# Optimization experiments

Hardware: AMD Instinct MI355X
Metric: run time of the kernel (lower is better)

Reference implementation:

```python
import jax, jax.numpy as jnp
import numpy as np

N_NODES = 100000
N_EDGES = 1600000
IN_DIM = 128
HID_DIM = 128
OUT_DIM = 64


def gcn_conv(x, W, b, edge_index):
    """GCNConv with add_self_loops, symmetric degree norm, add-aggregation.

    Math matches PyG: out[i] = sum_{(j,i) in E+selfloops} norm_ji * (x_j @ W) + b
    Since lin is linear and there is no edge_attr, we transform x once before
    the gather instead of per-edge (identical result, far less FLOPs/traffic).
    """
    n = x.shape[0]
    loop = jnp.arange(n, dtype=edge_index.dtype)
    row = jnp.concatenate([edge_index[0], loop])  # source nodes (x_j)
    col = jnp.concatenate([edge_index[1], loop])  # destination nodes
    # degree over destinations (includes self loops -> deg >= 1, no div by 0)
    deg = jax.ops.segment_sum(jnp.ones_like(col, dtype=x.dtype), col, num_segments=n)
    dinv = jax.lax.rsqrt(deg)
    norm = dinv[row] * dinv[col]  # [E+N]
    h = x @ W  # [N, out] transform once
    msg = norm[:, None] * h[row]  # [E+N, out] gathered per-edge messages
    out = jax.ops.segment_sum(msg, col, num_segments=n)  # scatter-add
    return out + b


def setup_inputs() -> dict:
    key = jax.random.key(0)
    k1, k2, k3, k4 = jax.random.split(key, 4)
    x = jax.random.normal(k1, (N_NODES, IN_DIM), dtype=jnp.float32)
    edge_index = jax.random.randint(k2, (2, N_EDGES), 0, N_NODES, dtype=jnp.int64)
    # glorot-ish init
    W1 = jax.random.normal(k3, (IN_DIM, HID_DIM), dtype=jnp.float32) * (2.0 / (IN_DIM + HID_DIM)) ** 0.5
    W2 = jax.random.normal(k4, (HID_DIM, OUT_DIM), dtype=jnp.float32) * (2.0 / (HID_DIM + OUT_DIM)) ** 0.5
    b1 = jnp.zeros((HID_DIM,), dtype=jnp.float32)
    b2 = jnp.zeros((OUT_DIM,), dtype=jnp.float32)
    return {"x": x, "edge_index": edge_index, "W1": W1, "b1": b1, "W2": W2, "b2": b2}


def reference(x, edge_index, W1, b1, W2, b2):
    # GCN.forward with prompt_type=None, pooling=False, eval mode (dropout is identity)
    h = gcn_conv(x, W1, b1, edge_index)
    h = jax.nn.relu(h)
    out = gcn_conv(h, W2, b2, edge_index)
    return out
```

## Files before the change

### kernel.cpp

```cpp
#include <hip/hip_runtime.h>


#define DIN 128
#define DHID 128
#define DOUT 64
#define ELLW 64
#define GPART 8
#define BPG 256

typedef __attribute__((ext_vector_type(4))) float f32x4;
typedef __attribute__((ext_vector_type(8))) short bf16x8;

__device__ __forceinline__ float bf2f(unsigned int u16) {
    return __uint_as_float(u16 << 16);
}
__device__ __forceinline__ unsigned short f2bf(float f) {
    unsigned int u = __float_as_uint(f);
    u += 0x7fffu + ((u >> 16) & 1u);
    return (unsigned short)(u >> 16);
}
__device__ __forceinline__ unsigned int pack2(float a, float b) {
    return (unsigned int)f2bf(a) | ((unsigned int)f2bf(b) << 16);
}

__global__ __launch_bounds__(256) void k_fill(const int* __restrict__ rows,
                                              const int* __restrict__ cols,
                                              int* __restrict__ deg,
                                              int* __restrict__ ell,
                                              int E, int perBlock, int R) {
    int g  = blockIdx.x & (GPART - 1);
    int cb = blockIdx.x >> 3;
    int lo = g * R, hi = lo + R;
    int eBeg = cb * perBlock;
    int eEnd = eBeg + perBlock; if (eEnd > E) eEnd = E;
    for (int e = eBeg + threadIdx.x; e < eEnd; e += 256) {
        int c = cols[e];
        if (c >= lo && c < hi) {
            int r = rows[e];
            int k = atomicAdd(&deg[c], 1);
            if (k < ELLW) ell[(size_t)c * ELLW + k] = r;
        }
    }
}

__global__ void k_dinv(const int* __restrict__ deg, float* __restrict__ dinv, int N) {
    int i = blockIdx.x * blockDim.x + threadIdx.x;
    if (i < N) dinv[i] = rsqrtf((float)(deg[i] + 1));
}

__global__ __launch_bounds__(256) void k_packW(const float* __restrict__ W1,
                                               const float* __restrict__ W2,
                                               unsigned short* __restrict__ w1p,
                                               unsigned short* __restrict__ w2p) {
    int id = blockIdx.x * 256 + threadIdx.x;
    if (id < 2048) {
        int lane = id & 63, s = (id >> 6) & 3, t = id >> 8;
        int n = t * 16 + (lane & 15);
        int k0 = s * 32 + (lane >> 4) * 8;
#pragma unroll
        for (int j = 0; j < 8; ++j)
            w1p[(size_t)id * 8 + j] = f2bf(W1[(k0 + j) * DHID + n]);
    } else if (id < 3072) {
        int id2 = id - 2048;
        int lane = id2 & 63, s = (id2 >> 6) & 3, t = id2 >> 8;
        int n = t * 16 + (lane & 15);
        int k0 = s * 32 + (lane >> 4) * 8;
#pragma unroll
        for (int j = 0; j < 8; ++j)
            w2p[(size_t)id2 * 8 + j] = f2bf(W2[(k0 + j) * DOUT + n]);
    }
}

__global__ __launch_bounds__(256) void k_gemm1(const float* __restrict__ x,
                                               const unsigned short* __restrict__ w1p,
                                               unsigned short* __restrict__ h1b, int N) {
    int wave = threadIdx.x >> 6, lane = threadIdx.x & 63;
    int quad = lane >> 4, qr = lane & 15;
    int rowBase = blockIdx.x * 64 + wave * 16;
    int arow = rowBase + qr;
    bool rowOK = arow < N;
    f32x4 acc[8] = {};
#pragma unroll
    for (int s = 0; s < 4; ++s) {
        bf16x8 a = {};
        if (rowOK) {
            const float* ap = x + (size_t)arow * DIN + s * 32 + quad * 8;
            float4 lo = *(const float4*)ap;
            float4 hi = *(const float4*)(ap + 4);
            a[0] = (short)f2bf(lo.x); a[1] = (short)f2bf(lo.y);
            a[2] = (short)f2bf(lo.z); a[3] = (short)f2bf(lo.w);
            a[4] = (short)f2bf(hi.x); a[5] = (short)f2bf(hi.y);
            a[6] = (short)f2bf(hi.z); a[7] = (short)f2bf(hi.w);
        }
#pragma unroll
        for (int t = 0; t < 8; ++t) {
            bf16x8 b = *(const bf16x8*)(w1p + ((size_t)(t * 4 + s) * 64 + lane) * 8);
            acc[t] = __builtin_amdgcn_mfma_f32_16x16x32_bf16(a, b, acc[t], 0, 0, 0);
        }
    }
#pragma unroll
    for (int t = 0; t < 8; ++t)
#pragma unroll
        for (int i = 0; i < 4; ++i) {
            int r = rowBase + quad * 4 + i;
            if (r < N) h1b[(size_t)r * DHID + t * 16 + qr] = f2bf(acc[t][i]);
        }
}

__global__ __launch_bounds__(256) void k_gather1(const int* __restrict__ deg,
                                                 const int* __restrict__ ell,
                                                 const float* __restrict__ dinv,
                                                 const unsigned int* __restrict__ h1u,
                                                 const float* __restrict__ b1,
                                                 unsigned int* __restrict__ hactu, int N) {
    int w = (blockIdx.x * 256 + threadIdx.x) >> 6;
    int lane = threadIdx.x & 63;
    if (w >= N) return;
    int d = deg[w]; if (d > ELLW) d = ELLW;
    int iv = ell[(size_t)w * ELLW + lane];
    float dv = (lane < d) ? dinv[iv] : 0.f;
    float a0 = 0.f, a1 = 0.f;
    int e = 0;
    for (; e + 4 <= d; e += 4) {
        int s0 = __shfl(iv, e + 0), s1 = __shfl(iv, e + 1);
        int s2 = __shfl(iv, e + 2), s3 = __shfl(iv, e + 3);
        float w0 = __shfl(dv, e + 0), w1 = __shfl(dv, e + 1);
        float w2 = __shfl(dv, e + 2), w3 = __shfl(dv, e + 3);
        unsigned int v0 = h1u[(size_t)s0 * 64 + lane];
        unsigned int v1 = h1u[(size_t)s1 * 64 + lane];
        unsigned int v2 = h1u[(size_t)s2 * 64 + lane];
        unsigned int v3 = h1u[(size_t)s3 * 64 + lane];
        a0 = fmaf(w0, bf2f(v0 & 0xffffu), a0); a1 = fmaf(w0, bf2f(v0 >> 16), a1);
        a0 = fmaf(w1, bf2f(v1 & 0xffffu), a0); a1 = fmaf(w1, bf2f(v1 >> 16), a1);
        a0 = fmaf(w2, bf2f(v2 & 0xffffu), a0); a1 = fmaf(w2, bf2f(v2 >> 16), a1);
        a0 = fmaf(w3, bf2f(v3 & 0xffffu), a0); a1 = fmaf(w3, bf2f(v3 >> 16), a1);
    }
    for (; e < d; ++e) {
        int s0 = __shfl(iv, e);
        float w0 = __shfl(dv, e);
        unsigned int v0 = h1u[(size_t)s0 * 64 + lane];
        a0 = fmaf(w0, bf2f(v0 & 0xffffu), a0); a1 = fmaf(w0, bf2f(v0 >> 16), a1);
    }
    float di = dinv[w], self = di * di;
    unsigned int hv = h1u[(size_t)w * 64 + lane];
    float2 bv = *(const float2*)(b1 + 2 * lane);
    float r0 = fmaf(di, a0, fmaf(self, bf2f(hv & 0xffffu), bv.x));
    float r1 = fmaf(di, a1, fmaf(self, bf2f(hv >> 16), bv.y));
    hactu[(size_t)w * 64 + lane] = pack2(fmaxf(r0, 0.f), fmaxf(r1, 0.f));
}

__global__ __launch_bounds__(256) void k_gemm2(const unsigned short* __restrict__ hactb,
                                               const unsigned short* __restrict__ w2p,
                                               unsigned short* __restrict__ h2b, int N) {
    int wave = threadIdx.x >> 6, lane = threadIdx.x & 63;
    int quad = lane >> 4, qr = lane & 15;
    int rowBase = blockIdx.x * 64 + wave * 16;
    int arow = rowBase + qr;
    bool rowOK = arow < N;
    f32x4 acc[4] = {};
#pragma unroll
    for (int s = 0; s < 4; ++s) {
        bf16x8 a = {};
        if (rowOK) a = *(const bf16x8*)(hactb + (size_t)arow * DHID + s * 32 + quad * 8);
#pragma unroll
        for (int t = 0; t < 4; ++t) {
            bf16x8 b = *(const bf16x8*)(w2p + ((size_t)(t * 4 + s) * 64 + lane) * 8);
            acc[t] = __builtin_amdgcn_mfma_f32_16x16x32_bf16(a, b, acc[t], 0, 0, 0);
        }
    }
#pragma unroll
    for (int t = 0; t < 4; ++t)
#pragma unroll
        for (int i = 0; i < 4; ++i) {
            int r = rowBase + quad * 4 + i;
            if (r < N) h2b[(size_t)r * DOUT + t * 16 + qr] = f2bf(acc[t][i]);
        }
}

__global__ __launch_bounds__(256) void k_gather2(const int* __restrict__ deg,
                                                 const int* __restrict__ ell,
                                                 const float* __restrict__ dinv,
                                                 const unsigned short* __restrict__ h2u,
                                                 const float* __restrict__ b2,
                                                 float* __restrict__ out, int N) {
    int w = (blockIdx.x * 256 + threadIdx.x) >> 6;
    int lane = threadIdx.x & 63;
    if (w >= N) return;
    int d = deg[w]; if (d > ELLW) d = ELLW;
    int iv = ell[(size_t)w * ELLW + lane];
    float dv = (lane < d) ? dinv[iv] : 0.f;
    float a = 0.f;
    int e = 0;
    for (; e + 4 <= d; e += 4) {
        int s0 = __shfl(iv, e + 0), s1 = __shfl(iv, e + 1);
        int s2 = __shfl(iv, e + 2), s3 = __shfl(iv, e + 3);
        float w0 = __shfl(dv, e + 0), w1 = __shfl(dv, e + 1);
        float w2 = __shfl(dv, e + 2), w3 = __shfl(dv, e + 3);
        float v0 = bf2f((unsigned int)h2u[(size_t)s0 * DOUT + lane]);
        float v1 = bf2f((unsigned int)h2u[(size_t)s1 * DOUT + lane]);
        float v2 = bf2f((unsigned int)h2u[(size_t)s2 * DOUT + lane]);
        float v3 = bf2f((unsigned int)h2u[(size_t)s3 * DOUT + lane]);
        a = fmaf(w0, v0, a); a = fmaf(w1, v1, a);
        a = fmaf(w2, v2, a); a = fmaf(w3, v3, a);
    }
    for (; e < d; ++e) {
        int s0 = __shfl(iv, e);
        float w0 = __shfl(dv, e);
        a = fmaf(w0, bf2f((unsigned int)h2u[(size_t)s0 * DOUT + lane]), a);
    }
    float di = dinv[w], self = di * di;
    float hv = bf2f((unsigned int)h2u[(size_t)w * DOUT + lane]);
    out[(size_t)w * DOUT + lane] = fmaf(di, a, fmaf(self, hv, b2[lane]));
}

extern "C" void kernel_launch(void* const* d_in, const int* in_sizes, int n_in,
                              void* d_out, int out_size, void* d_ws, size_t ws_size,
                              hipStream_t stream) {
    const float* x  = (const float*)d_in[0];
    const int*   ei = (const int*)d_in[1];
    const float* W1 = (const float*)d_in[2];
    const float* b1 = (const float*)d_in[3];
    const float* W2 = (const float*)d_in[4];
    const float* b2 = (const float*)d_in[5];

    const int N = in_sizes[0] / DIN;
    const int E = in_sizes[1] / 2;
    const int* rows = ei;
    const int* cols = ei + E;

    char* p = (char*)d_ws;
    int*   ell  = (int*)p;                  p += (size_t)N * ELLW * 4;
    unsigned short* h1b = (unsigned short*)p; p += (size_t)N * DHID * 2;
    unsigned short* hactb = (unsigned short*)p; p += (size_t)N * DHID * 2;
    unsigned short* w1p = (unsigned short*)p; p += (size_t)2048 * 8 * 2;
    unsigned short* w2p = (unsigned short*)p; p += (size_t)1024 * 8 * 2;
    int*   deg  = (int*)p;                  p += (size_t)N * 4;
    float* dinv = (float*)p;                p += (size_t)N * 4;
    unsigned short* h2b = h1b;

    const int R = (N + GPART - 1) / GPART;
    const int perBlock = (E + BPG - 1) / BPG;

    hipMemsetAsync(deg, 0, (size_t)N * 4, stream);
    k_fill<<<GPART * BPG, 256, 0, stream>>>(rows, cols, deg, ell, E, perBlock, R);
    k_dinv<<<(N + 255) / 256, 256, 0, stream>>>(deg, dinv, N);
    k_packW<<<12, 256, 0, stream>>>(W1, W2, w1p, w2p);

    k_gemm1<<<(N + 63) / 64, 256, 0, stream>>>(x, w1p, h1b, N);
    k_gather1<<<(N + 3) / 4, 256, 0, stream>>>(deg, ell, dinv, (const unsigned int*)h1b,
                                               b1, (unsigned int*)hactb, N);

    k_gemm2<<<(N + 63) / 64, 256, 0, stream>>>(hactb, w2p, h2b, N);
    k_gather2<<<(N + 3) / 4, 256, 0, stream>>>(deg, ell, dinv, h2b, b2, (float*)d_out, N);
}
```

Before: 321.5 us.

## Fuse ELL fill with first GEMM, drop dinv kernel, deepen gather unroll

Merges the edge-bucketing fill kernel and the first MFMA GEMM into one launch, with separate block ranges so the two independent stages can run concurrently. The fill now reads edges as int4 vectors, with perBlock rounded to a multiple of four. The dinv kernel and buffer are removed; gathers recompute rsqrt from deg on the fly, adding an extra dependent degree load per neighbor lane. The gather loops get an 8-wide unrolled stage to keep more independent row loads in flight, at the cost of more registers.

Measured after the change: 312.4 us. 2.8% less time.

```diff
diff --git a/kernel.cpp b/kernel.cpp
--- a/kernel.cpp
+++ b/kernel.cpp
@@ -21,31 +21,6 @@
 }
 __device__ __forceinline__ unsigned int pack2(float a, float b) {
     return (unsigned int)f2bf(a) | ((unsigned int)f2bf(b) << 16);
-}
-
-__global__ __launch_bounds__(256) void k_fill(const int* __restrict__ rows,
-                                              const int* __restrict__ cols,
-                                              int* __restrict__ deg,
-                                              int* __restrict__ ell,
-                                              int E, int perBlock, int R) {
-    int g  = blockIdx.x & (GPART - 1);
-    int cb = blockIdx.x >> 3;
-    int lo = g * R, hi = lo + R;
-    int eBeg = cb * perBlock;
-    int eEnd = eBeg + perBlock; if (eEnd > E) eEnd = E;
-    for (int e = eBeg + threadIdx.x; e < eEnd; e += 256) {
-        int c = cols[e];
-        if (c >= lo && c < hi) {
-            int r = rows[e];
-            int k = atomicAdd(&deg[c], 1);
-            if (k < ELLW) ell[(size_t)c * ELLW + k] = r;
-        }
-    }
-}
-
-__global__ void k_dinv(const int* __restrict__ deg, float* __restrict__ dinv, int N) {
-    int i = blockIdx.x * blockDim.x + threadIdx.x;
-    if (i < N) dinv[i] = rsqrtf((float)(deg[i] + 1));
 }
 
 __global__ __launch_bounds__(256) void k_packW(const float* __restrict__ W1,
@@ -71,12 +46,44 @@
     }
 }
 
-__global__ __launch_bounds__(256) void k_gemm1(const float* __restrict__ x,
-                                               const unsigned short* __restrict__ w1p,
-                                               unsigned short* __restrict__ h1b, int N) {
+__device__ __forceinline__ void fill_edge(int c, int r, int lo, int hi,
+                                          int* __restrict__ deg, int* __restrict__ ell) {
+    if (c >= lo && c < hi) {
+        int k = atomicAdd(&deg[c], 1);
+        if (k < ELLW) ell[(size_t)c * ELLW + k] = r;
+    }
+}
+
+__global__ __launch_bounds__(256) void k_fill_gemm1(
+        const int* __restrict__ rows, const int* __restrict__ cols,
+        int* __restrict__ deg, int* __restrict__ ell,
+        int E, int perBlock, int R, int FB,
+        const float* __restrict__ x, const unsigned short* __restrict__ w1p,
+        unsigned short* __restrict__ h1b, int N) {
+    if ((int)blockIdx.x < FB) {
+        int g  = blockIdx.x & (GPART - 1);
+        int cb = blockIdx.x >> 3;
+        int lo = g * R, hi = lo + R;
+        int eBeg = cb * perBlock;
+        int eEnd = eBeg + perBlock; if (eEnd > E) eEnd = E;
+        for (int e = eBeg + 4 * threadIdx.x; e < eEnd; e += 4 * 256) {
+            if (e + 3 < eEnd) {
+                int4 c4 = *(const int4*)(cols + e);
+                int4 r4 = *(const int4*)(rows + e);
+                fill_edge(c4.x, r4.x, lo, hi, deg, ell);
+                fill_edge(c4.y, r4.y, lo, hi, deg, ell);
+                fill_edge(c4.z, r4.z, lo, hi, deg, ell);
+                fill_edge(c4.w, r4.w, lo, hi, deg, ell);
+            } else {
+                for (int j = e; j < eEnd; ++j) fill_edge(cols[j], rows[j], lo, hi, deg, ell);
+            }
+        }
+        return;
+    }
+    int bid = blockIdx.x - FB;
     int wave = threadIdx.x >> 6, lane = threadIdx.x & 63;
     int quad = lane >> 4, qr = lane & 15;
-    int rowBase = blockIdx.x * 64 + wave * 16;
+    int rowBase = bid * 64 + wave * 16;
     int arow = rowBase + qr;
     bool rowOK = arow < N;
     f32x4 acc[8] = {};
@@ -109,7 +116,6 @@
 
 __global__ __launch_bounds__(256) void k_gather1(const int* __restrict__ deg,
                                                  const int* __restrict__ ell,
-                                                 const float* __restrict__ dinv,
                                                  const unsigned int* __restrict__ h1u,
                                                  const float* __restrict__ b1,
                                                  unsigned int* __restrict__ hactu, int N) {
@@ -118,22 +124,32 @@
     if (w >= N) return;
     int d = deg[w]; if (d > ELLW) d = ELLW;
     int iv = ell[(size_t)w * ELLW + lane];
-    float dv = (lane < d) ? dinv[iv] : 0.f;
+    float dv = (lane < d) ? rsqrtf((float)(deg[iv] + 1)) : 0.f;
     float a0 = 0.f, a1 = 0.f;
     int e = 0;
+    for (; e + 8 <= d; e += 8) {
+        int s[8]; float wg[8]; unsigned int v[8];
+#pragma unroll
+        for (int j = 0; j < 8; ++j) { s[j] = __shfl(iv, e + j); wg[j] = __shfl(dv, e + j); }
+#pragma unroll
+        for (int j = 0; j < 8; ++j) v[j] = h1u[(size_t)s[j] * 64 + lane];
+#pragma unroll
+        for (int j = 0; j < 8; ++j) {
+            a0 = fmaf(wg[j], bf2f(v[j] & 0xffffu), a0);
+            a1 = fmaf(wg[j], bf2f(v[j] >> 16), a1);
+        }
+    }
     for (; e + 4 <= d; e += 4) {
-        int s0 = __shfl(iv, e + 0), s1 = __shfl(iv, e + 1);
-        int s2 = __shfl(iv, e + 2), s3 = __shfl(iv, e + 3);
-        float w0 = __shfl(dv, e + 0), w1 = __shfl(dv, e + 1);
-        float w2 = __shfl(dv, e + 2), w3 = __shfl(dv, e + 3);
-        unsigned int v0 = h1u[(size_t)s0 * 64 + lane];
-        unsigned int v1 = h1u[(size_t)s1 * 64 + lane];
-        unsigned int v2 = h1u[(size_t)s2 * 64 + lane];
-        unsigned int v3 = h1u[(size_t)s3 * 64 + lane];
-        a0 = fmaf(w0, bf2f(v0 & 0xffffu), a0); a1 = fmaf(w0, bf2f(v0 >> 16), a1);
-        a0 = fmaf(w1, bf2f(v1 & 0xffffu), a0); a1 = fmaf(w1, bf2f(v1 >> 16), a1);
-        a0 = fmaf(w2, bf2f(v2 & 0xffffu), a0); a1 = fmaf(w2, bf2f(v2 >> 16), a1);
-        a0 = fmaf(w3, bf2f(v3 & 0xffffu), a0); a1 = fmaf(w3, bf2f(v3 >> 16), a1);
+        int s[4]; float wg[4]; unsigned int v[4];
+#pragma unroll
+        for (int j = 0; j < 4; ++j) { s[j] = __shfl(iv, e + j); wg[j] = __shfl(dv, e + j); }
+#pragma unroll
+        for (int j = 0; j < 4; ++j) v[j] = h1u[(size_t)s[j] * 64 + lane];
+#pragma unroll
+        for (int j = 0; j < 4; ++j) {
+            a0 = fmaf(wg[j], bf2f(v[j] & 0xffffu), a0);
+            a1 = fmaf(wg[j], bf2f(v[j] >> 16), a1);
+        }
     }
     for (; e < d; ++e) {
         int s0 = __shfl(iv, e);
@@ -141,7 +157,7 @@
         unsigned int v0 = h1u[(size_t)s0 * 64 + lane];
         a0 = fmaf(w0, bf2f(v0 & 0xffffu), a0); a1 = fmaf(w0, bf2f(v0 >> 16), a1);
     }
-    float di = dinv[w], self = di * di;
+    float di = rsqrtf((float)(d + 1)), self = di * di;
     unsigned int hv = h1u[(size_t)w * 64 + lane];
     float2 bv = *(const float2*)(b1 + 2 * lane);
     float r0 = fmaf(di, a0, fmaf(self, bf2f(hv & 0xffffu), bv.x));
@@ -179,7 +195,6 @@
 
 __global__ __launch_bounds__(256) void k_gather2(const int* __restrict__ deg,
                                                  const int* __restrict__ ell,
-                                                 const float* __restrict__ dinv,
                                                  const unsigned short* __restrict__ h2u,
                                                  const float* __restrict__ b2,
                                                  float* __restrict__ out, int N) {
@@ -188,27 +203,33 @@
     if (w >= N) return;
     int d = deg[w]; if (d > ELLW) d = ELLW;
     int iv = ell[(size_t)w * ELLW + lane];
-    float dv = (lane < d) ? dinv[iv] : 0.f;
+    float dv = (lane < d) ? rsqrtf((float)(deg[iv] + 1)) : 0.f;
     float a = 0.f;
     int e = 0;
+    for (; e + 8 <= d; e += 8) {
+        int s[8]; float wg[8]; float v[8];
+#pragma unroll
+        for (int j = 0; j < 8; ++j) { s[j] = __shfl(iv, e + j); wg[j] = __shfl(dv, e + j); }
+#pragma unroll
+        for (int j = 0; j < 8; ++j) v[j] = bf2f((unsigned int)h2u[(size_t)s[j] * DOUT + lane]);
+#pragma unroll
+        for (int j = 0; j < 8; ++j) a = fmaf(wg[j], v[j], a);
+    }
     for (; e + 4 <= d; e += 4) {
-        int s0 = __shfl(iv, e + 0), s1 = __shfl(iv, e + 1);
-        int s2 = __shfl(iv, e + 2), s3 = __shfl(iv, e + 3);
-        float w0 = __shfl(dv, e + 0), w1 = __shfl(dv, e + 1);
-        float w2 = __shfl(dv, e + 2), w3 = __shfl(dv, e + 3);
-        float v0 = bf2f((unsigned int)h2u[(size_t)s0 * DOUT + lane]);
-        float v1 = bf2f((unsigned int)h2u[(size_t)s1 * DOUT + lane]);
-        float v2 = bf2f((unsigned int)h2u[(size_t)s2 * DOUT + lane]);
-        float v3 = bf2f((unsigned int)h2u[(size_t)s3 * DOUT + lane]);
-        a = fmaf(w0, v0, a); a = fmaf(w1, v1, a);
-        a = fmaf(w2, v2, a); a = fmaf(w3, v3, a);
+        int s[4]; float wg[4]; float v[4];
+#pragma unroll
+        for (int j = 0; j < 4; ++j) { s[j] = __shfl(iv, e + j); wg[j] = __shfl(dv, e + j); }
+#pragma unroll
+        for (int j = 0; j < 4; ++j) v[j] = bf2f((unsigned int)h2u[(size_t)s[j] * DOUT + lane]);
+#pragma unroll
+        for (int j = 0; j < 4; ++j) a = fmaf(wg[j], v[j], a);
     }
     for (; e < d; ++e) {
         int s0 = __shfl(iv, e);
         float w0 = __shfl(dv, e);
         a = fmaf(w0, bf2f((unsigned int)h2u[(size_t)s0 * DOUT + lane]), a);
     }
-    float di = dinv[w], self = di * di;
+    float di = rsqrtf((float)(d + 1)), self = di * di;
     float hv = bf2f((unsigned int)h2u[(size_t)w * DOUT + lane]);
     out[(size_t)w * DOUT + lane] = fmaf(di, a, fmaf(self, hv, b2[lane]));
 }
@@ -229,27 +250,29 @@
     const int* cols = ei + E;
 
     char* p = (char*)d_ws;
-    int*   ell  = (int*)p;                  p += (size_t)N * ELLW * 4;
-    unsigned short* h1b = (unsigned short*)p; p += (size_t)N * DHID * 2;
+    int*   ell  = (int*)p;                    p += (size_t)N * ELLW * 4;
+    unsigned short* h1b = (unsigned short*)p;   p += (size_t)N * DHID * 2;
     unsigned short* hactb = (unsigned short*)p; p += (size_t)N * DHID * 2;
-    unsigned short* w1p = (unsigned short*)p; p += (size_t)2048 * 8 * 2;
-    unsigned short* w2p = (unsigned short*)p; p += (size_t)1024 * 8 * 2;
-    int*   deg  = (int*)p;                  p += (size_t)N * 4;
-    float* dinv = (float*)p;                p += (size_t)N * 4;
+    unsigned short* w1p = (unsigned short*)p;   p += (size_t)2048 * 8 * 2;
+    unsigned short* w2p = (unsigned short*)p;   p += (size_t)1024 * 8 * 2;
+    int*   deg  = (int*)p;                    p += (size_t)N * 4;
     unsigned short* h2b = h1b;
 
     const int R = (N + GPART - 1) / GPART;
-    const int perBlock = (E + BPG - 1) / BPG;
-
+    int perBlock = (E + BPG - 1) / BPG;
+    perBlock = (perBlock + 3) & ~3;
+    const int FB = GPART * BPG;
+    const int GB = (N + 63) / 64;
+
+    k_packW<<<12, 256, 0, stream>>>(W1, W2, w1p, w2p);
     hipMemsetAsync(deg, 0, (size_t)N * 4, stream);
-    k_fill<<<GPART * BPG, 256, 0, stream>>>(rows, cols, deg, ell, E, perBlock, R);
-    k_dinv<<<(N + 255) / 256, 256, 0, stream>>>(deg, dinv, N);
-    k_packW<<<12, 256, 0, stream>>>(W1, W2, w1p, w2p);
-
-    k_gemm1<<<(N + 63) / 64, 256, 0, stream>>>(x, w1p, h1b, N);
-    k_gather1<<<(N + 3) / 4, 256, 0, stream>>>(deg, ell, dinv, (const unsigned int*)h1b,
+
+    k_fill_gemm1<<<FB + GB, 256, 0, stream>>>(rows, cols, deg, ell, E, perBlock, R, FB,
+                                              x, w1p, h1b, N);
+
+    k_gather1<<<(N + 3) / 4, 256, 0, stream>>>(deg, ell, (const unsigned int*)h1b,
                                                b1, (unsigned int*)hactb, N);
 
     k_gemm2<<<(N + 63) / 64, 256, 0, stream>>>(hactb, w2p, h2b, N);
-    k_gather2<<<(N + 3) / 4, 256, 0, stream>>>(deg, ell, dinv, h2b, b2, (float*)d_out, N);
-}
+    k_gather2<<<(N + 3) / 4, 256, 0, stream>>>(deg, ell, h2b, b2, (float*)d_out, N);
+}
```
